# Optimization experiments

Measured on AMD Instinct MI355X. Metric: run time of the kernel, lower is better.

## Reference

```python
import jax, jax.numpy as jnp
import numpy as np

B = 4096  # number of graphs (segments)
H = 256   # hidden_aff = hidden_comp = hidden_prot
NEG = -1e30

def leaky(x):
    return jax.nn.leaky_relu(x, 0.1)

def _lin(key, fin, fout):
    k1, k2 = jax.random.split(key)
    lim = 1.0 / np.sqrt(fin)
    W = jax.random.uniform(k1, (fin, fout), jnp.float32, -lim, lim)
    b = jax.random.uniform(k2, (fout,), jnp.float32, -lim, lim)
    return W, b

def setup_inputs() -> dict:
    key = jax.random.key(0)
    ks = jax.random.split(key, 16)
    N = 262144
    comp_feature = jax.random.normal(ks[0], (N, H), jnp.float32)
    prot_feature = jax.random.normal(ks[1], (N, H), jnp.float32)
    batch_comp = jnp.sort(jax.random.randint(ks[2], (N,), 0, B, jnp.int32))
    batch_prot = jnp.sort(jax.random.randint(ks[3], (N,), 0, B, jnp.int32))
    c_aff_W, c_aff_b = _lin(ks[4], H, H)
    c_sup_W, c_sup_b = _lin(ks[5], H, H)
    p_aff_W, p_aff_b = _lin(ks[6], H, H)
    raw_W1, raw_b1 = _lin(ks[7], 3 * H, H)
    raw_W2, raw_b2 = _lin(ks[8], H, H)
    alpha_W1, alpha_b1 = _lin(ks[9], 3 * H, H)
    alpha_W2, alpha_b2 = _lin(ks[10], H, 1)
    out_W1, out_b1 = _lin(ks[11], H, H)
    out_W2, out_b2 = _lin(ks[12], H, 1)
    return dict(comp_feature=comp_feature, prot_feature=prot_feature,
                batch_comp=batch_comp, batch_prot=batch_prot,
                c_aff_W=c_aff_W, c_aff_b=c_aff_b, c_sup_W=c_sup_W, c_sup_b=c_sup_b,
                p_aff_W=p_aff_W, p_aff_b=p_aff_b,
                raw_W1=raw_W1, raw_b1=raw_b1, raw_W2=raw_W2, raw_b2=raw_b2,
                alpha_W1=alpha_W1, alpha_b1=alpha_b1, alpha_W2=alpha_W2, alpha_b2=alpha_b2,
                out_W1=out_W1, out_b1=out_b1, out_W2=out_W2, out_b2=out_b2)

def reference(comp_feature, prot_feature, batch_comp, batch_prot,
              c_aff_W, c_aff_b, c_sup_W, c_sup_b, p_aff_W, p_aff_b,
              raw_W1, raw_b1, raw_W2, raw_b2,
              alpha_W1, alpha_b1, alpha_W2, alpha_b2,
              out_W1, out_b1, out_W2, out_b2):
    comp_emb = leaky(comp_feature @ c_aff_W + c_aff_b)           # [N, H]
    prot_emb = leaky(prot_feature @ p_aff_W + p_aff_b)           # [N, H]
    prot_pool = jax.ops.segment_max(prot_emb, batch_prot, num_segments=B)  # [B, H]
    supe = jax.ops.segment_sum(leaky(comp_feature @ c_sup_W + c_sup_b),
                               batch_comp, num_segments=B)       # [B, H]
    feat = jnp.concatenate([comp_emb, supe[batch_comp], prot_pool[batch_comp]], axis=1)  # [N, 3H]
    raw = leaky(feat @ raw_W1 + raw_b1) @ raw_W2 + raw_b2        # [N, H]
    prealpha = leaky(feat @ alpha_W1 + alpha_b1) @ alpha_W2 + alpha_b2  # [N, 1]
    # scatter softmax over graphs
    seg_max = jax.ops.segment_max(prealpha, batch_comp, num_segments=B)
    a_exp = jnp.exp(prealpha - seg_max[batch_comp])
    a_sum = jax.ops.segment_sum(a_exp, batch_comp, num_segments=B) + 1e-6
    alpha = a_exp / a_sum[batch_comp]                            # [N, 1]
    vector = jax.ops.segment_sum(raw * alpha, batch_comp, num_segments=B)  # [B, H]
    affinity_pred = leaky(vector @ out_W1 + out_b1) @ out_W2 + out_b2      # [B, 1]
    return vector, alpha, affinity_pred
```

## Files before the change

kernel.cpp:

```cpp
#include <hip/hip_runtime.h>
#include <cstddef>
#include <cstdint>

#define HDIM 256
#define BSEG 4096

typedef __bf16 bf16x8 __attribute__((ext_vector_type(8)));
typedef float f32x4 __attribute__((ext_vector_type(4)));

__device__ __forceinline__ float leaky(float x) { return x >= 0.f ? x : 0.1f * x; }
__device__ __forceinline__ float bf2f(ushort u) {
    return __builtin_bit_cast(float, (uint32_t)u << 16);
}
__device__ __forceinline__ ushort f2bf(float f) {
    uint32_t x = __builtin_bit_cast(uint32_t, f);
    return (ushort)((x + 0x7fffu + ((x >> 16) & 1u)) >> 16);
}
__device__ __forceinline__ bf16x8 pack8(float4 a, float4 b) {
    union { ushort s[8]; bf16x8 v; } u;
    u.s[0] = f2bf(a.x); u.s[1] = f2bf(a.y); u.s[2] = f2bf(a.z); u.s[3] = f2bf(a.w);
    u.s[4] = f2bf(b.x); u.s[5] = f2bf(b.y); u.s[6] = f2bf(b.z); u.s[7] = f2bf(b.w);
    return u.v;
}
__device__ __forceinline__ void store_bf4(ushort* p, float v0, float v1, float v2, float v3) {
    ushort4 o; o.x = f2bf(v0); o.y = f2bf(v1); o.z = f2bf(v2); o.w = f2bf(v3);
    *(ushort4*)p = o;
}

__device__ __forceinline__ void gld16(const ushort* g, ushort* lds) {
    __builtin_amdgcn_global_load_lds(
        (const __attribute__((address_space(1))) uint32_t*)g,
        (__attribute__((address_space(3))) uint32_t*)lds, 16, 0, 0);
}

__global__ void seg_bounds_k(const int* __restrict__ bc, const int* __restrict__ bp,
                             int* __restrict__ sc, int* __restrict__ sp, int n, int nb)
{
    int t = blockIdx.x * blockDim.x + threadIdx.x;
    if (t >= 2 * (nb + 1)) return;
    bool isc = (t <= nb);
    const int* a = isc ? bc : bp;
    int v = isc ? t : t - (nb + 1);
    int lo = 0, hi = n;
    while (lo < hi) { int mid = (lo + hi) >> 1; if (a[mid] < v) lo = mid + 1; else hi = mid; }
    if (isc) sc[t] = lo; else sp[t - (nb + 1)] = lo;
}

__global__ __launch_bounds__(256) void wt_cast_all(
    const float* __restrict__ s0, const float* __restrict__ s1,
    const float* __restrict__ s2, const float* __restrict__ s3,
    const float* __restrict__ s4,
    ushort* __restrict__ d0, ushort* __restrict__ d1, ushort* __restrict__ d2,
    ushort* __restrict__ d3, ushort* __restrict__ d4)
{
    int m = blockIdx.x >> 4, tile = blockIdx.x & 15;
    const float* s = m == 0 ? s0 : m == 1 ? s1 : m == 2 ? s2 : m == 3 ? s3 : s4;
    ushort*      d = m == 0 ? d0 : m == 1 ? d1 : m == 2 ? d2 : m == 3 ? d3 : d4;
    int r0 = (tile >> 2) * 64, c0 = (tile & 3) * 64;
    __shared__ ushort t[64][72];
    int cc = threadIdx.x & 63, rr = threadIdx.x >> 6;
    for (int r = rr; r < 64; r += 4) t[cc][r] = f2bf(s[(size_t)(r0 + r) * 256 + c0 + cc]);
    __syncthreads();
    for (int r = rr; r < 64; r += 4) d[(size_t)(c0 + r) * 256 + r0 + cc] = t[r][cc];
}

template<bool LEAKYACT, bool ROWBIAS, bool AFP32, bool ALPHADOT, int YT>
__global__ __launch_bounds__(512) void mg3(
    const void* __restrict__ Av, const ushort* __restrict__ WT,
    const float* __restrict__ bias0, const float* __restrict__ bias1,
    const float* __restrict__ rt0, const float* __restrict__ rt1,
    const int* __restrict__ idx,
    ushort* __restrict__ out0, ushort* __restrict__ out1,
    const float* __restrict__ w2, float* __restrict__ pre)
{
    __shared__ __attribute__((aligned(16))) ushort Bs[2][256 * 32];
    __shared__ __attribute__((aligned(16))) ushort As[2][128 * 32];
    __shared__ float pb[128][4];

    const int tid = threadIdx.x;
    const int l = tid & 63, w = tid >> 6;

    const uint nwg = gridDim.x, orig = blockIdx.x;
    const uint swz = (orig & 7) * (nwg >> 3) + (orig >> 3);
    const int bx = (int)(swz / YT), cb = (int)(swz % YT);
    const int row0 = bx * 128, colb = cb * 256;

    const float*  Af = (const float*)Av;
    const ushort* Ah = (const ushort*)Av;

    const int sB0 = w * 128 + l;
    const int rB0 = sB0 >> 2,        rB1 = (sB0 + 64) >> 2;
    const int qB0 = (sB0 & 3) ^ ((rB0 >> 1) & 3), qB1 = ((sB0 + 64) & 3) ^ ((rB1 >> 1) & 3);
    const ushort* srcB0 = WT + (size_t)(colb + rB0) * HDIM + qB0 * 8;
    const ushort* srcB1 = WT + (size_t)(colb + rB1) * HDIM + qB1 * 8;
    const int srow = tid >> 2, sj = tid & 3;
    const int lj = sj ^ ((srow >> 1) & 3);
    const float*  fsrcA = Af + (size_t)(row0 + srow) * HDIM + lj * 8;
    const ushort* hsrcA = Ah + (size_t)(row0 + srow) * HDIM + lj * 8;

    const int wr = (w >> 2) * 64, wc = (w & 3) * 64;
    const int lr = l & 15, lt = l >> 4;

    f32x4 acc[4][4] = {};

#define STAGE_B(buf, k0) do { \
        gld16(srcB0 + (k0), &Bs[buf][sB0 * 8]); \
        gld16(srcB1 + (k0), &Bs[buf][(sB0 + 64) * 8]); \
    } while (0)

#define COMPUTE(buf) do { \
        bf16x8 af[4], bv[4]; \
        _Pragma("unroll") \
        for (int m = 0; m < 4; ++m) { \
            const int row = wr + m * 16 + lr; \
            const int q = lt ^ ((row >> 1) & 3); \
            af[m] = *(const bf16x8*)&As[buf][row * 32 + q * 8]; \
        } \
        _Pragma("unroll") \
        for (int n = 0; n < 4; ++n) { \
            const int brow = wc + n * 16 + lr; \
            const int q = lt ^ ((brow >> 1) & 3); \
            bv[n] = *(const bf16x8*)&Bs[buf][brow * 32 + q * 8]; \
        } \
        _Pragma("unroll") \
        for (int m = 0; m < 4; ++m) \
            _Pragma("unroll") \
            for (int n = 0; n < 4; ++n) \
                acc[m][n] = __builtin_amdgcn_mfma_f32_16x16x32_bf16(bv[n], af[m], acc[m][n], 0, 0, 0); \
    } while (0)

    int cur = 0;
    if (AFP32) {
        float4 av0, av1;
        av0 = *(const float4*)(fsrcA + 0);
        av1 = *(const float4*)(fsrcA + 4);
        STAGE_B(0, 0);
        *(bf16x8*)&As[0][tid * 8] = pack8(av0, av1);
        __syncthreads();
        #pragma unroll
        for (int t = 1; t < 8; ++t) {
            av0 = *(const float4*)(fsrcA + t * 32);
            av1 = *(const float4*)(fsrcA + t * 32 + 4);
            STAGE_B(cur ^ 1, t * 32);
            COMPUTE(cur);
            *(bf16x8*)&As[cur ^ 1][tid * 8] = pack8(av0, av1);
            __syncthreads();
            cur ^= 1;
        }
        COMPUTE(cur);
    } else {
        STAGE_B(0, 0);
        gld16(hsrcA, &As[0][tid * 8]);
        __syncthreads();
        #pragma unroll
        for (int t = 1; t < 8; ++t) {
            STAGE_B(cur ^ 1, t * 32);
            gld16(hsrcA + t * 32, &As[cur ^ 1][tid * 8]);
            COMPUTE(cur);
            __syncthreads();
            cur ^= 1;
        }
        COMPUTE(cur);
    }

#undef STAGE_B
#undef COMPUTE

    if (ALPHADOT && cb == 1) {
        #pragma unroll
        for (int m = 0; m < 4; ++m) {
            const int row = row0 + wr + m * 16 + lr;
            const float* rrow = rt1 + (size_t)idx[row] * HDIM;
            float p = 0.f;
            #pragma unroll
            for (int n = 0; n < 4; ++n) {
                const int c = wc + n * 16 + (lt << 2);
                float4 r4 = *(const float4*)&rrow[c];
                float4 w4 = *(const float4*)&w2[c];
                float v0 = acc[m][n][0] + r4.x, v1 = acc[m][n][1] + r4.y;
                float v2 = acc[m][n][2] + r4.z, v3 = acc[m][n][3] + r4.w;
                if (LEAKYACT) { v0 = leaky(v0); v1 = leaky(v1); v2 = leaky(v2); v3 = leaky(v3); }
                p += v0 * w4.x + v1 * w4.y + v2 * w4.z + v3 * w4.w;
            }
            p += __shfl_xor(p, 16);
            p += __shfl_xor(p, 32);
            if (lt == 0) pb[wr + m * 16 + lr][w & 3] = p;
        }
        __syncthreads();
        if (tid < 128) pre[row0 + tid] = pb[tid][0] + pb[tid][1] + pb[tid][2] + pb[tid][3];
    } else {
        const float* bias = (YT == 2 && cb == 1) ? bias1 : bias0;
        const float* rtab = (YT == 2 && cb == 1) ? rt1 : rt0;
        ushort* outp = (YT == 2 && cb == 1) ? out1 : out0;
        #pragma unroll
        for (int m = 0; m < 4; ++m) {
            const int row = row0 + wr + m * 16 + lr;
            const float* rrow = nullptr;
            if (ROWBIAS) rrow = rtab + (size_t)idx[row] * HDIM;
            #pragma unroll
            for (int n = 0; n < 4; ++n) {
                const int c = wc + n * 16 + (lt << 2);
                float v0 = acc[m][n][0], v1 = acc[m][n][1], v2 = acc[m][n][2], v3 = acc[m][n][3];
                if (bias) {
                    float4 b4 = *(const float4*)&bias[c];
                    v0 += b4.x; v1 += b4.y; v2 += b4.z; v3 += b4.w;
                }
                if (ROWBIAS) {
                    float4 r4 = *(const float4*)&rrow[c];
                    v0 += r4.x; v1 += r4.y; v2 += r4.z; v3 += r4.w;
                }
                if (LEAKYACT) { v0 = leaky(v0); v1 = leaky(v1); v2 = leaky(v2); v3 = leaky(v3); }
                store_bf4(&outp[(size_t)row * HDIM + c], v0, v1, v2, v3);
            }
        }
    }
}

__global__ __launch_bounds__(256) void gemm64_2(
    const float* __restrict__ A, const float* __restrict__ A2,
    const float* __restrict__ Wb_r, const float* __restrict__ Wc_r, const float* __restrict__ bias_r,
    const float* __restrict__ Wb_a, const float* __restrict__ Wc_a, const float* __restrict__ bias_a,
    float* __restrict__ Cr, float* __restrict__ Ca)
{
    const int K = HDIM, NO = HDIM;
    const float* W  = blockIdx.z ? Wb_a : Wb_r;
    const float* W2 = blockIdx.z ? Wc_a : Wc_r;
    const float* bias = blockIdx.z ? bias_a : bias_r;
    float* C = blockIdx.z ? Ca : Cr;

    __shared__ float As [16][68];
    __shared__ float Bs [16][68];
    __shared__ float As2[16][68];
    __shared__ float Bs2[16][68];

    const int tid = threadIdx.x;
    const int tx = tid & 15, ty = tid >> 4;
    const int row0 = blockIdx.x * 64, col0 = blockIdx.y * 64;

    const int lr = tid >> 2;
    const int lk = (tid & 3) << 2;
    const int bk = tid >> 4;
    const int bj = (tid & 15) << 2;

    float acc[4][4] = {};

    for (int k0 = 0; k0 < K; k0 += 16) {
        float4 a4 = *(const float4*)&A[(size_t)(row0 + lr) * K + k0 + lk];
        As[lk + 0][lr] = a4.x; As[lk + 1][lr] = a4.y;
        As[lk + 2][lr] = a4.z; As[lk + 3][lr] = a4.w;
        *(float4*)&Bs[bk][bj] = *(const float4*)&W[(size_t)(k0 + bk) * NO + col0 + bj];
        float4 c4 = *(const float4*)&A2[(size_t)(row0 + lr) * K + k0 + lk];
        As2[lk + 0][lr] = c4.x; As2[lk + 1][lr] = c4.y;
        As2[lk + 2][lr] = c4.z; As2[lk + 3][lr] = c4.w;
        *(float4*)&Bs2[bk][bj] = *(const float4*)&W2[(size_t)(k0 + bk) * NO + col0 + bj];
        __syncthreads();
        #pragma unroll
        for (int kk = 0; kk < 16; ++kk) {
            float4 av = *(const float4*)&As[kk][ty << 2];
            float4 bv = *(const float4*)&Bs[kk][tx << 2];
            float a_[4] = {av.x, av.y, av.z, av.w};
            float b_[4] = {bv.x, bv.y, bv.z, bv.w};
            #pragma unroll
            for (int i = 0; i < 4; ++i)
                #pragma unroll
                for (int j = 0; j < 4; ++j)
                    acc[i][j] += a_[i] * b_[j];
            float4 av2 = *(const float4*)&As2[kk][ty << 2];
            float4 bv2 = *(const float4*)&Bs2[kk][tx << 2];
            float c_[4] = {av2.x, av2.y, av2.z, av2.w};
            float d_[4] = {bv2.x, bv2.y, bv2.z, bv2.w};
            #pragma unroll
            for (int i = 0; i < 4; ++i)
                #pragma unroll
                for (int j = 0; j < 4; ++j)
                    acc[i][j] += c_[i] * d_[j];
        }
        __syncthreads();
    }

    #pragma unroll
    for (int i = 0; i < 4; ++i) {
        int row = row0 + (ty << 2) + i;
        float vv[4];
        #pragma unroll
        for (int j = 0; j < 4; ++j) {
            int col = col0 + (tx << 2) + j;
            vv[j] = acc[i][j] + bias[col];
        }
        float4 o; o.x = vv[0]; o.y = vv[1]; o.z = vv[2]; o.w = vv[3];
        *(float4*)&C[(size_t)row * NO + col0 + (tx << 2)] = o;
    }
}

template<bool ISMAX>
__global__ __launch_bounds__(256) void seg_reduce8(const ushort* __restrict__ in,
        const int* __restrict__ starts, float* __restrict__ out)
{
    __shared__ float part[8][HDIM];
    const int b = blockIdx.x, tid = threadIdx.x;
    const int sub = tid & 31, r = tid >> 5;
    const int s = starts[b], e = starts[b + 1];
    float a[8];
    #pragma unroll
    for (int j = 0; j < 8; ++j) a[j] = ISMAX ? -INFINITY : 0.f;
    for (int i = s + r; i < e; i += 8) {
        uint4 v = *(const uint4*)&in[(size_t)i * HDIM + sub * 8];
        float f[8] = { bf2f((ushort)v.x), bf2f((ushort)(v.x >> 16)),
                       bf2f((ushort)v.y), bf2f((ushort)(v.y >> 16)),
                       bf2f((ushort)v.z), bf2f((ushort)(v.z >> 16)),
                       bf2f((ushort)v.w), bf2f((ushort)(v.w >> 16)) };
        #pragma unroll
        for (int j = 0; j < 8; ++j) a[j] = ISMAX ? fmaxf(a[j], f[j]) : (a[j] + f[j]);
    }
    #pragma unroll
    for (int j = 0; j < 8; ++j) part[r][sub * 8 + j] = a[j];
    __syncthreads();
    float res = part[0][tid];
    #pragma unroll
    for (int j = 1; j < 8; ++j) res = ISMAX ? fmaxf(res, part[j][tid]) : (res + part[j][tid]);
    out[(size_t)b * HDIM + tid] = res;
}

__global__ __launch_bounds__(64) void seg_softmax_k(const float* __restrict__ pre,
        const int* __restrict__ starts, float* __restrict__ alpha, float* __restrict__ sa)
{
    int b = blockIdx.x, lane = threadIdx.x;
    int s = starts[b], e = starts[b + 1];
    float m = -INFINITY;
    for (int i = s + lane; i < e; i += 64) m = fmaxf(m, pre[i]);
    #pragma unroll
    for (int off = 32; off; off >>= 1) m = fmaxf(m, __shfl_xor(m, off));
    float S = 0.f;
    for (int i = s + lane; i < e; i += 64) S += expf(pre[i] - m);
    #pragma unroll
    for (int off = 32; off; off >>= 1) S += __shfl_xor(S, off);
    float denom = S + 1e-6f;
    if (lane == 0) sa[b] = S / denom;
    for (int i = s + lane; i < e; i += 64) alpha[i] = expf(pre[i] - m) / denom;
}

__global__ __launch_bounds__(256) void seg_wsum8(const ushort* __restrict__ raw,
        const float* __restrict__ alpha, const int* __restrict__ starts,
        float* __restrict__ vec)
{
    __shared__ float part[8][HDIM];
    const int b = blockIdx.x, tid = threadIdx.x;
    const int sub = tid & 31, r = tid >> 5;
    const int s = starts[b], e = starts[b + 1];
    float a[8] = {};
    for (int i = s + r; i < e; i += 8) {
        float al = alpha[i];
        uint4 v = *(const uint4*)&raw[(size_t)i * HDIM + sub * 8];
        a[0] += bf2f((ushort)v.x) * al;        a[1] += bf2f((ushort)(v.x >> 16)) * al;
        a[2] += bf2f((ushort)v.y) * al;        a[3] += bf2f((ushort)(v.y >> 16)) * al;
        a[4] += bf2f((ushort)v.z) * al;        a[5] += bf2f((ushort)(v.z >> 16)) * al;
        a[6] += bf2f((ushort)v.w) * al;        a[7] += bf2f((ushort)(v.w >> 16)) * al;
    }
    #pragma unroll
    for (int j = 0; j < 8; ++j) part[r][sub * 8 + j] = a[j];
    __syncthreads();
    float res = 0.f;
    #pragma unroll
    for (int j = 0; j < 8; ++j) res += part[j][tid];
    vec[(size_t)b * HDIM + tid] = res;
}

__global__ __launch_bounds__(256) void final_k(
    const float* __restrict__ hw, const float* __restrict__ sa,
    const float* __restrict__ W2r, const float* __restrict__ rb2,
    const float* __restrict__ oW1, const float* __restrict__ ob1,
    const float* __restrict__ oW2, const float* __restrict__ ob2,
    float* __restrict__ out_vec, float* __restrict__ out_aff)
{
    __shared__ float v[HDIM];
    __shared__ float vecs[HDIM];
    __shared__ float red[4];
    int b = blockIdx.x, t = threadIdx.x;
    v[t] = hw[(size_t)b * HDIM + t];
    __syncthreads();
    float a = rb2[t] * sa[b];
    #pragma unroll 8
    for (int k = 0; k < HDIM; ++k) a += v[k] * W2r[(size_t)k * HDIM + t];
    out_vec[(size_t)b * HDIM + t] = a;
    vecs[t] = a;
    __syncthreads();
    float h = ob1[t];
    #pragma unroll 8
    for (int k = 0; k < HDIM; ++k) h += vecs[k] * oW1[(size_t)k * HDIM + t];
    h = leaky(h);
    float p = h * oW2[t];
    #pragma unroll
    for (int off = 32; off; off >>= 1) p += __shfl_down(p, off);
    int lane = t & 63, wid = t >> 6;
    if (lane == 0) red[wid] = p;
    __syncthreads();
    if (t == 0) out_aff[b] = red[0] + red[1] + red[2] + red[3] + ob2[0];
}

extern "C" void kernel_launch(void* const* d_in, const int* in_sizes, int n_in,
                              void* d_out, int out_size, void* d_ws, size_t ws_size,
                              hipStream_t stream)
{
    const int N = in_sizes[2];
    const int H = HDIM;
    const int B = BSEG;

    const float* comp   = (const float*)d_in[0];
    const float* prot   = (const float*)d_in[1];
    const int*   bc     = (const int*)d_in[2];
    const int*   bp     = (const int*)d_in[3];
    const float* c_aff_W = (const float*)d_in[4];
    const float* c_aff_b = (const float*)d_in[5];
    const float* c_sup_W = (const float*)d_in[6];
    const float* c_sup_b = (const float*)d_in[7];
    const float* p_aff_W = (const float*)d_in[8];
    const float* p_aff_b = (const float*)d_in[9];
    const float* raw_W1  = (const float*)d_in[10];
    const float* raw_b1  = (const float*)d_in[11];
    const float* raw_W2  = (const float*)d_in[12];
    const float* raw_b2  = (const float*)d_in[13];
    const float* alpha_W1 = (const float*)d_in[14];
    const float* alpha_b1 = (const float*)d_in[15];
    const float* alpha_W2 = (const float*)d_in[16];
    const float* out_W1  = (const float*)d_in[18];
    const float* out_b1  = (const float*)d_in[19];
    const float* out_W2  = (const float*)d_in[20];
    const float* out_b2  = (const float*)d_in[21];

    const size_t NBIG = (size_t)N * H;
    const size_t SSEG = (size_t)B * H;

    char* p = (char*)d_ws;
    ushort* e1 = (ushort*)p; p += NBIG * 2;
    ushort* e2 = (ushort*)p; p += NBIG * 2;
    ushort* e3 = (ushort*)p; p += NBIG * 2;
    float* supe = (float*)p;  p += SSEG * 4;
    float* pool = (float*)p;  p += SSEG * 4;
    float* gr   = (float*)p;  p += SSEG * 4;
    float* ga   = (float*)p;  p += SSEG * 4;
    float* hw   = (float*)p;  p += SSEG * 4;
    float* sa   = (float*)p;  p += (size_t)B * 4;
    float* pre  = (float*)p;  p += (size_t)N * 4;
    ushort* WT1 = (ushort*)p; p += (size_t)512 * 256 * 2;
    ushort* WTp = (ushort*)p; p += (size_t)256 * 256 * 2;
    ushort* WT2 = (ushort*)p; p += (size_t)512 * 256 * 2;
    int* sc = (int*)p; p += (size_t)(B + 1) * 4;
    int* sp = (int*)p; p += (size_t)(B + 1) * 4;
    if ((size_t)(p - (char*)d_ws) > ws_size) return;

    ushort* h1 = e3;

    float* out_vec   = (float*)d_out;
    float* out_alpha = out_vec + SSEG;
    float* out_aff   = out_alpha + N;

    dim3 blk(256), blk5(512);

    seg_bounds_k<<<(2 * (B + 1) + 255) / 256, blk, 0, stream>>>(bc, bp, sc, sp, N, B);
    wt_cast_all<<<5 * 16, blk, 0, stream>>>(
        c_aff_W, c_sup_W, p_aff_W, raw_W1, alpha_W1,
        WT1, WT1 + 65536, WTp, WT2, WT2 + 65536);

    mg3<true, false, true, false, 2><<<dim3(N / 128 * 2), blk5, 0, stream>>>(
        comp, WT1, c_aff_b, c_sup_b, nullptr, nullptr, nullptr, e1, e2, nullptr, nullptr);
    mg3<true, false, true, false, 1><<<dim3(N / 128), blk5, 0, stream>>>(
        prot, WTp, p_aff_b, nullptr, nullptr, nullptr, nullptr, e3, nullptr, nullptr, nullptr);
    seg_reduce8<false><<<B, blk, 0, stream>>>(e2, sc, supe);
    seg_reduce8<true ><<<B, blk, 0, stream>>>(e3, sp, pool);
    gemm64_2<<<dim3(B / 64, 4, 2), blk, 0, stream>>>(supe, pool,
        raw_W1 + H * H, raw_W1 + 2 * H * H, raw_b1,
        alpha_W1 + H * H, alpha_W1 + 2 * H * H, alpha_b1, gr, ga);
    mg3<true, true, false, true, 2><<<dim3(N / 128 * 2), blk5, 0, stream>>>(
        e1, WT2, nullptr, nullptr, gr, ga, bc, h1, nullptr, alpha_W2, pre);
    seg_softmax_k<<<B, dim3(64), 0, stream>>>(pre, sc, out_alpha, sa);
    seg_wsum8<<<B, blk, 0, stream>>>(h1, out_alpha, sc, hw);
    final_k<<<B, blk, 0, stream>>>(hw, sa, raw_W2, raw_b2,
        out_W1, out_b1, out_W2, out_b2, out_vec, out_aff);
}
```

Measured before the change: 686.3 us.

## Enlarge GEMM row tile to 256 rows per block with 8x4 MFMA accumulators

Doubles the M tile of the MFMA GEMM kernel from 128 to 256 rows, so each wave computes 128x64 outputs (8x4 accumulator tiles) and each loaded B tile is reused across twice as many rows. A staging now uses two 16-byte slots per thread, and the grid is halved. The aim is higher arithmetic intensity and less redundant weight traffic. The cost is more registers (128 accumulator floats) and more LDS, which lowers occupancy and may cause spilling.

Result: slower. 700.2 us (+2.0%).

```diff
diff --git a/kernel.cpp b/kernel.cpp
--- a/kernel.cpp
+++ b/kernel.cpp
@@ -65,7 +65,7 @@
 }
 
 template<bool LEAKYACT, bool ROWBIAS, bool AFP32, bool ALPHADOT, int YT>
-__global__ __launch_bounds__(512) void mg3(
+__global__ __launch_bounds__(512) void mg8(
     const void* __restrict__ Av, const ushort* __restrict__ WT,
     const float* __restrict__ bias0, const float* __restrict__ bias1,
     const float* __restrict__ rt0, const float* __restrict__ rt1,
@@ -74,8 +74,8 @@
     const float* __restrict__ w2, float* __restrict__ pre)
 {
     __shared__ __attribute__((aligned(16))) ushort Bs[2][256 * 32];
-    __shared__ __attribute__((aligned(16))) ushort As[2][128 * 32];
-    __shared__ float pb[128][4];
+    __shared__ __attribute__((aligned(16))) ushort As[2][256 * 32];
+    __shared__ float pb[256][4];
 
     const int tid = threadIdx.x;
     const int l = tid & 63, w = tid >> 6;
@@ -83,35 +83,57 @@
     const uint nwg = gridDim.x, orig = blockIdx.x;
     const uint swz = (orig & 7) * (nwg >> 3) + (orig >> 3);
     const int bx = (int)(swz / YT), cb = (int)(swz % YT);
-    const int row0 = bx * 128, colb = cb * 256;
+    const int row0 = bx * 256, colb = cb * 256;
 
     const float*  Af = (const float*)Av;
     const ushort* Ah = (const ushort*)Av;
 
-    const int sB0 = w * 128 + l;
-    const int rB0 = sB0 >> 2,        rB1 = (sB0 + 64) >> 2;
-    const int qB0 = (sB0 & 3) ^ ((rB0 >> 1) & 3), qB1 = ((sB0 + 64) & 3) ^ ((rB1 >> 1) & 3);
+    const int s0 = tid, s1 = tid + 512;
+    const int rB0 = s0 >> 2, rB1 = s1 >> 2;
+    const int qB0 = (s0 & 3) ^ ((rB0 >> 1) & 3), qB1 = (s1 & 3) ^ ((rB1 >> 1) & 3);
     const ushort* srcB0 = WT + (size_t)(colb + rB0) * HDIM + qB0 * 8;
     const ushort* srcB1 = WT + (size_t)(colb + rB1) * HDIM + qB1 * 8;
-    const int srow = tid >> 2, sj = tid & 3;
-    const int lj = sj ^ ((srow >> 1) & 3);
-    const float*  fsrcA = Af + (size_t)(row0 + srow) * HDIM + lj * 8;
-    const ushort* hsrcA = Ah + (size_t)(row0 + srow) * HDIM + lj * 8;
-
-    const int wr = (w >> 2) * 64, wc = (w & 3) * 64;
+    const int rA0 = s0 >> 2, rA1 = s1 >> 2;
+    const int qA0 = (s0 & 3) ^ ((rA0 >> 1) & 3), qA1 = (s1 & 3) ^ ((rA1 >> 1) & 3);
+    const float*  fsrcA0 = Af + (size_t)(row0 + rA0) * HDIM + qA0 * 8;
+    const float*  fsrcA1 = Af + (size_t)(row0 + rA1) * HDIM + qA1 * 8;
+    const ushort* hsrcA0 = Ah + (size_t)(row0 + rA0) * HDIM + qA0 * 8;
+    const ushort* hsrcA1 = Ah + (size_t)(row0 + rA1) * HDIM + qA1 * 8;
+
+    const int wr = (w >> 2) * 128, wc = (w & 3) * 64;
     const int lr = l & 15, lt = l >> 4;
 
-    f32x4 acc[4][4] = {};
+    f32x4 acc[8][4] = {};
+    float4 fa[4];
+    bf16x8 hb[2];
+    (void)hb;
 
 #define STAGE_B(buf, k0) do { \
-        gld16(srcB0 + (k0), &Bs[buf][sB0 * 8]); \
-        gld16(srcB1 + (k0), &Bs[buf][(sB0 + 64) * 8]); \
+        gld16(srcB0 + (k0), &Bs[buf][s0 * 8]); \
+        gld16(srcB1 + (k0), &Bs[buf][s1 * 8]); \
     } while (0)
 
+#define LOAD_A_F(k0) do { \
+        fa[0] = *(const float4*)(fsrcA0 + (k0)); \
+        fa[1] = *(const float4*)(fsrcA0 + (k0) + 4); \
+        fa[2] = *(const float4*)(fsrcA1 + (k0)); \
+        fa[3] = *(const float4*)(fsrcA1 + (k0) + 4); \
+    } while (0)
+
+#define WRITE_A(buf) do { \
+        *(bf16x8*)&As[buf][s0 * 8] = pack8(fa[0], fa[1]); \
+        *(bf16x8*)&As[buf][s1 * 8] = pack8(fa[2], fa[3]); \
+    } while (0)
+
+#define STAGE_A_H(buf, k0) do { \
+        gld16(hsrcA0 + (k0), &As[buf][s0 * 8]); \
+        gld16(hsrcA1 + (k0), &As[buf][s1 * 8]); \
+    } while (0)
+
 #define COMPUTE(buf) do { \
-        bf16x8 af[4], bv[4]; \
+        bf16x8 af[8], bv[4]; \
         _Pragma("unroll") \
-        for (int m = 0; m < 4; ++m) { \
+        for (int m = 0; m < 8; ++m) { \
             const int row = wr + m * 16 + lr; \
             const int q = lt ^ ((row >> 1) & 3); \
             af[m] = *(const bf16x8*)&As[buf][row * 32 + q * 8]; \
@@ -123,52 +145,44 @@
             bv[n] = *(const bf16x8*)&Bs[buf][brow * 32 + q * 8]; \
         } \
         _Pragma("unroll") \
-        for (int m = 0; m < 4; ++m) \
+        for (int m = 0; m < 8; ++m) \
             _Pragma("unroll") \
             for (int n = 0; n < 4; ++n) \
                 acc[m][n] = __builtin_amdgcn_mfma_f32_16x16x32_bf16(bv[n], af[m], acc[m][n], 0, 0, 0); \
     } while (0)
 
-    int cur = 0;
     if (AFP32) {
-        float4 av0, av1;
-        av0 = *(const float4*)(fsrcA + 0);
-        av1 = *(const float4*)(fsrcA + 4);
+        LOAD_A_F(0);
         STAGE_B(0, 0);
-        *(bf16x8*)&As[0][tid * 8] = pack8(av0, av1);
+        WRITE_A(0);
         __syncthreads();
         #pragma unroll
-        for (int t = 1; t < 8; ++t) {
-            av0 = *(const float4*)(fsrcA + t * 32);
-            av1 = *(const float4*)(fsrcA + t * 32 + 4);
-            STAGE_B(cur ^ 1, t * 32);
-            COMPUTE(cur);
-            *(bf16x8*)&As[cur ^ 1][tid * 8] = pack8(av0, av1);
-            __syncthreads();
-            cur ^= 1;
-        }
-        COMPUTE(cur);
+        for (int t = 0; t < 8; ++t) {
+            if (t < 7) { STAGE_B((t + 1) & 1, (t + 1) * 32); LOAD_A_F((t + 1) * 32); }
+            COMPUTE(t & 1);
+            if (t < 7) { WRITE_A((t + 1) & 1); __syncthreads(); }
+        }
     } else {
         STAGE_B(0, 0);
-        gld16(hsrcA, &As[0][tid * 8]);
+        STAGE_A_H(0, 0);
         __syncthreads();
         #pragma unroll
-        for (int t = 1; t < 8; ++t) {
-            STAGE_B(cur ^ 1, t * 32);
-            gld16(hsrcA + t * 32, &As[cur ^ 1][tid * 8]);
-            COMPUTE(cur);
-            __syncthreads();
-            cur ^= 1;
-        }
-        COMPUTE(cur);
+        for (int t = 0; t < 8; ++t) {
+            if (t < 7) { STAGE_B((t + 1) & 1, (t + 1) * 32); STAGE_A_H((t + 1) & 1, (t + 1) * 32); }
+            COMPUTE(t & 1);
+            if (t < 7) __syncthreads();
+        }
     }
 
 #undef STAGE_B
+#undef LOAD_A_F
+#undef WRITE_A
+#undef STAGE_A_H
 #undef COMPUTE
 
     if (ALPHADOT && cb == 1) {
         #pragma unroll
-        for (int m = 0; m < 4; ++m) {
+        for (int m = 0; m < 8; ++m) {
             const int row = row0 + wr + m * 16 + lr;
             const float* rrow = rt1 + (size_t)idx[row] * HDIM;
             float p = 0.f;
@@ -187,13 +201,13 @@
             if (lt == 0) pb[wr + m * 16 + lr][w & 3] = p;
         }
         __syncthreads();
-        if (tid < 128) pre[row0 + tid] = pb[tid][0] + pb[tid][1] + pb[tid][2] + pb[tid][3];
+        if (tid < 256) pre[row0 + tid] = pb[tid][0] + pb[tid][1] + pb[tid][2] + pb[tid][3];
     } else {
         const float* bias = (YT == 2 && cb == 1) ? bias1 : bias0;
         const float* rtab = (YT == 2 && cb == 1) ? rt1 : rt0;
         ushort* outp = (YT == 2 && cb == 1) ? out1 : out0;
         #pragma unroll
-        for (int m = 0; m < 4; ++m) {
+        for (int m = 0; m < 8; ++m) {
             const int row = row0 + wr + m * 16 + lr;
             const float* rrow = nullptr;
             if (ROWBIAS) rrow = rtab + (size_t)idx[row] * HDIM;
@@ -461,16 +475,16 @@
         c_aff_W, c_sup_W, p_aff_W, raw_W1, alpha_W1,
         WT1, WT1 + 65536, WTp, WT2, WT2 + 65536);
 
-    mg3<true, false, true, false, 2><<<dim3(N / 128 * 2), blk5, 0, stream>>>(
+    mg8<true, false, true, false, 2><<<dim3(N / 256 * 2), blk5, 0, stream>>>(
         comp, WT1, c_aff_b, c_sup_b, nullptr, nullptr, nullptr, e1, e2, nullptr, nullptr);
-    mg3<true, false, true, false, 1><<<dim3(N / 128), blk5, 0, stream>>>(
+    mg8<true, false, true, false, 1><<<dim3(N / 256), blk5, 0, stream>>>(
         prot, WTp, p_aff_b, nullptr, nullptr, nullptr, nullptr, e3, nullptr, nullptr, nullptr);
     seg_reduce8<false><<<B, blk, 0, stream>>>(e2, sc, supe);
     seg_reduce8<true ><<<B, blk, 0, stream>>>(e3, sp, pool);
     gemm64_2<<<dim3(B / 64, 4, 2), blk, 0, stream>>>(supe, pool,
         raw_W1 + H * H, raw_W1 + 2 * H * H, raw_b1,
         alpha_W1 + H * H, alpha_W1 + 2 * H * H, alpha_b1, gr, ga);
-    mg3<true, true, false, true, 2><<<dim3(N / 128 * 2), blk5, 0, stream>>>(
+    mg8<true, true, false, true, 2><<<dim3(N / 256 * 2), blk5, 0, stream>>>(
         e1, WT2, nullptr, nullptr, gr, ga, bc, h1, nullptr, alpha_W2, pre);
     seg_softmax_k<<<B, dim3(64), 0, stream>>>(pre, sc, out_alpha, sa);
     seg_wsum8<<<B, blk, 0, stream>>>(h1, out_alpha, sc, hw);
```

## Fuse comp_emb GEMM into raw/alpha GEMM, keeping embedding tile in LDS

Applied to the files above, without the earlier changes.

Comp_emb is no longer written to global memory as e1 and read back. A new fused kernel computes the comp_aff GEMM per 128-row tile, stores the leaky bf16 result in shared memory, then runs both the raw and alpha second-layer GEMMs from LDS. This removes a full N×H bf16 write and read. The cost is that comp_feature is re-read (the sup GEMM now runs separately), B operands are read directly from global without LDS staging, and the kernel uses a large LDS footprint (about 80KB), which lowers occupancy.

Result: slower. 790.2 us (+15.1%).

```diff
diff --git a/kernel.cpp b/kernel.cpp
--- a/kernel.cpp
+++ b/kernel.cpp
@@ -64,18 +64,14 @@
     for (int r = rr; r < 64; r += 4) d[(size_t)(c0 + r) * 256 + r0 + cc] = t[r][cc];
 }
 
-template<bool LEAKYACT, bool ROWBIAS, bool AFP32, bool ALPHADOT, int YT>
+template<bool LEAKYACT, bool AFP32, int YT>
 __global__ __launch_bounds__(512) void mg3(
     const void* __restrict__ Av, const ushort* __restrict__ WT,
-    const float* __restrict__ bias0, const float* __restrict__ bias1,
-    const float* __restrict__ rt0, const float* __restrict__ rt1,
-    const int* __restrict__ idx,
-    ushort* __restrict__ out0, ushort* __restrict__ out1,
-    const float* __restrict__ w2, float* __restrict__ pre)
+    const float* __restrict__ bias0,
+    ushort* __restrict__ out0)
 {
     __shared__ __attribute__((aligned(16))) ushort Bs[2][256 * 32];
     __shared__ __attribute__((aligned(16))) ushort As[2][128 * 32];
-    __shared__ float pb[128][4];
 
     const int tid = threadIdx.x;
     const int l = tid & 63, w = tid >> 6;
@@ -84,6 +80,7 @@
     const uint swz = (orig & 7) * (nwg >> 3) + (orig >> 3);
     const int bx = (int)(swz / YT), cb = (int)(swz % YT);
     const int row0 = bx * 128, colb = cb * 256;
+    (void)colb;
 
     const float*  Af = (const float*)Av;
     const ushort* Ah = (const ushort*)Av;
@@ -166,21 +163,169 @@
 #undef STAGE_B
 #undef COMPUTE
 
-    if (ALPHADOT && cb == 1) {
+    #pragma unroll
+    for (int m = 0; m < 4; ++m) {
+        const int row = row0 + wr + m * 16 + lr;
+        #pragma unroll
+        for (int n = 0; n < 4; ++n) {
+            const int c = wc + n * 16 + (lt << 2);
+            float v0 = acc[m][n][0], v1 = acc[m][n][1], v2 = acc[m][n][2], v3 = acc[m][n][3];
+            float4 b4 = *(const float4*)&bias0[c];
+            v0 += b4.x; v1 += b4.y; v2 += b4.z; v3 += b4.w;
+            if (LEAKYACT) { v0 = leaky(v0); v1 = leaky(v1); v2 = leaky(v2); v3 = leaky(v3); }
+            store_bf4(&out0[(size_t)row * HDIM + c], v0, v1, v2, v3);
+        }
+    }
+}
+
+__global__ __launch_bounds__(512) void mgfused(
+    const float* __restrict__ Af, const ushort* __restrict__ WTa,
+    const float* __restrict__ abias,
+    const ushort* __restrict__ WT2,
+    const float* __restrict__ gr, const float* __restrict__ ga,
+    const int* __restrict__ idx, const float* __restrict__ w2,
+    ushort* __restrict__ h1, float* __restrict__ pre)
+{
+    __shared__ __attribute__((aligned(16))) ushort As[2][128 * 32];
+    __shared__ __attribute__((aligned(16))) ushort eL[8][128 * 32];
+    float (*pb)[4] = (float (*)[4])As;
+
+    const int tid = threadIdx.x;
+    const int l = tid & 63, w = tid >> 6;
+    const uint nwg = gridDim.x, orig = blockIdx.x;
+    const uint swz = (orig & 7) * (nwg >> 3) + (orig >> 3);
+    const int row0 = (int)swz * 128;
+
+    const int srow = tid >> 2, sj = tid & 3;
+    const int lj = sj ^ ((srow >> 1) & 3);
+    const float* fsrcA = Af + (size_t)(row0 + srow) * HDIM + lj * 8;
+
+    const int wr = (w >> 2) * 64, wc = (w & 3) * 64;
+    const int lr = l & 15, lt = l >> 4;
+
+    f32x4 acc[4][4] = {};
+
+    {
+        float4 av0 = *(const float4*)(fsrcA);
+        float4 av1 = *(const float4*)(fsrcA + 4);
+        *(bf16x8*)&As[0][tid * 8] = pack8(av0, av1);
+        __syncthreads();
+        #pragma unroll
+        for (int t = 0; t < 8; ++t) {
+            if (t < 7) {
+                av0 = *(const float4*)(fsrcA + (t + 1) * 32);
+                av1 = *(const float4*)(fsrcA + (t + 1) * 32 + 4);
+            }
+            bf16x8 af[4], bv[4];
+            #pragma unroll
+            for (int m = 0; m < 4; ++m) {
+                const int row = wr + m * 16 + lr;
+                const int q = lt ^ ((row >> 1) & 3);
+                af[m] = *(const bf16x8*)&As[t & 1][row * 32 + q * 8];
+            }
+            #pragma unroll
+            for (int n = 0; n < 4; ++n)
+                bv[n] = *(const bf16x8*)&WTa[(size_t)(wc + n * 16 + lr) * HDIM + t * 32 + lt * 8];
+            #pragma unroll
+            for (int m = 0; m < 4; ++m)
+                #pragma unroll
+                for (int n = 0; n < 4; ++n)
+                    acc[m][n] = __builtin_amdgcn_mfma_f32_16x16x32_bf16(bv[n], af[m], acc[m][n], 0, 0, 0);
+            if (t < 7) {
+                *(bf16x8*)&As[(t + 1) & 1][tid * 8] = pack8(av0, av1);
+                __syncthreads();
+            }
+        }
+    }
+    #pragma unroll
+    for (int m = 0; m < 4; ++m) {
+        const int r = wr + m * 16 + lr;
+        #pragma unroll
+        for (int n = 0; n < 4; ++n) {
+            const int c = wc + n * 16 + (lt << 2);
+            float4 b4 = *(const float4*)&abias[c];
+            float v0 = leaky(acc[m][n][0] + b4.x);
+            float v1 = leaky(acc[m][n][1] + b4.y);
+            float v2 = leaky(acc[m][n][2] + b4.z);
+            float v3 = leaky(acc[m][n][3] + b4.w);
+            const int ks = c >> 5, o = c & 31;
+            const int s = (o >> 3) ^ ((r >> 1) & 3);
+            ushort4 u; u.x = f2bf(v0); u.y = f2bf(v1); u.z = f2bf(v2); u.w = f2bf(v3);
+            *(ushort4*)&eL[ks][r * 32 + s * 8 + (o & 7)] = u;
+        }
+    }
+    __syncthreads();
+
+    {
+        f32x4 hacc[4][4] = {};
+        #pragma unroll
+        for (int ks = 0; ks < 8; ++ks) {
+            bf16x8 af[4], bv[4];
+            #pragma unroll
+            for (int m = 0; m < 4; ++m) {
+                const int row = wr + m * 16 + lr;
+                const int q = lt ^ ((row >> 1) & 3);
+                af[m] = *(const bf16x8*)&eL[ks][row * 32 + q * 8];
+            }
+            #pragma unroll
+            for (int n = 0; n < 4; ++n)
+                bv[n] = *(const bf16x8*)&WT2[(size_t)(wc + n * 16 + lr) * HDIM + ks * 32 + lt * 8];
+            #pragma unroll
+            for (int m = 0; m < 4; ++m)
+                #pragma unroll
+                for (int n = 0; n < 4; ++n)
+                    hacc[m][n] = __builtin_amdgcn_mfma_f32_16x16x32_bf16(bv[n], af[m], hacc[m][n], 0, 0, 0);
+        }
         #pragma unroll
         for (int m = 0; m < 4; ++m) {
             const int row = row0 + wr + m * 16 + lr;
-            const float* rrow = rt1 + (size_t)idx[row] * HDIM;
+            const float* rrow = gr + (size_t)idx[row] * HDIM;
+            #pragma unroll
+            for (int n = 0; n < 4; ++n) {
+                const int c = wc + n * 16 + (lt << 2);
+                float4 r4 = *(const float4*)&rrow[c];
+                store_bf4(&h1[(size_t)row * HDIM + c],
+                          leaky(hacc[m][n][0] + r4.x), leaky(hacc[m][n][1] + r4.y),
+                          leaky(hacc[m][n][2] + r4.z), leaky(hacc[m][n][3] + r4.w));
+            }
+        }
+    }
+
+    {
+        f32x4 aacc[4][4] = {};
+        #pragma unroll
+        for (int ks = 0; ks < 8; ++ks) {
+            bf16x8 af[4], bv[4];
+            #pragma unroll
+            for (int m = 0; m < 4; ++m) {
+                const int row = wr + m * 16 + lr;
+                const int q = lt ^ ((row >> 1) & 3);
+                af[m] = *(const bf16x8*)&eL[ks][row * 32 + q * 8];
+            }
+            #pragma unroll
+            for (int n = 0; n < 4; ++n)
+                bv[n] = *(const bf16x8*)&WT2[(size_t)(256 + wc + n * 16 + lr) * HDIM + ks * 32 + lt * 8];
+            #pragma unroll
+            for (int m = 0; m < 4; ++m)
+                #pragma unroll
+                for (int n = 0; n < 4; ++n)
+                    aacc[m][n] = __builtin_amdgcn_mfma_f32_16x16x32_bf16(bv[n], af[m], aacc[m][n], 0, 0, 0);
+        }
+        __syncthreads();
+        #pragma unroll
+        for (int m = 0; m < 4; ++m) {
+            const int row = row0 + wr + m * 16 + lr;
+            const float* rrow = ga + (size_t)idx[row] * HDIM;
             float p = 0.f;
             #pragma unroll
             for (int n = 0; n < 4; ++n) {
                 const int c = wc + n * 16 + (lt << 2);
                 float4 r4 = *(const float4*)&rrow[c];
                 float4 w4 = *(const float4*)&w2[c];
-                float v0 = acc[m][n][0] + r4.x, v1 = acc[m][n][1] + r4.y;
-                float v2 = acc[m][n][2] + r4.z, v3 = acc[m][n][3] + r4.w;
-                if (LEAKYACT) { v0 = leaky(v0); v1 = leaky(v1); v2 = leaky(v2); v3 = leaky(v3); }
-                p += v0 * w4.x + v1 * w4.y + v2 * w4.z + v3 * w4.w;
+                p += leaky(aacc[m][n][0] + r4.x) * w4.x;
+                p += leaky(aacc[m][n][1] + r4.y) * w4.y;
+                p += leaky(aacc[m][n][2] + r4.z) * w4.z;
+                p += leaky(aacc[m][n][3] + r4.w) * w4.w;
             }
             p += __shfl_xor(p, 16);
             p += __shfl_xor(p, 32);
@@ -188,31 +333,6 @@
         }
         __syncthreads();
         if (tid < 128) pre[row0 + tid] = pb[tid][0] + pb[tid][1] + pb[tid][2] + pb[tid][3];
-    } else {
-        const float* bias = (YT == 2 && cb == 1) ? bias1 : bias0;
-        const float* rtab = (YT == 2 && cb == 1) ? rt1 : rt0;
-        ushort* outp = (YT == 2 && cb == 1) ? out1 : out0;
-        #pragma unroll
-        for (int m = 0; m < 4; ++m) {
-            const int row = row0 + wr + m * 16 + lr;
-            const float* rrow = nullptr;
-            if (ROWBIAS) rrow = rtab + (size_t)idx[row] * HDIM;
-            #pragma unroll
-            for (int n = 0; n < 4; ++n) {
-                const int c = wc + n * 16 + (lt << 2);
-                float v0 = acc[m][n][0], v1 = acc[m][n][1], v2 = acc[m][n][2], v3 = acc[m][n][3];
-                if (bias) {
-                    float4 b4 = *(const float4*)&bias[c];
-                    v0 += b4.x; v1 += b4.y; v2 += b4.z; v3 += b4.w;
-                }
-                if (ROWBIAS) {
-                    float4 r4 = *(const float4*)&rrow[c];
-                    v0 += r4.x; v1 += r4.y; v2 += r4.z; v3 += r4.w;
-                }
-                if (LEAKYACT) { v0 = leaky(v0); v1 = leaky(v1); v2 = leaky(v2); v3 = leaky(v3); }
-                store_bf4(&outp[(size_t)row * HDIM + c], v0, v1, v2, v3);
-            }
-        }
     }
 }
 
@@ -431,7 +551,6 @@
     const size_t SSEG = (size_t)B * H;
 
     char* p = (char*)d_ws;
-    ushort* e1 = (ushort*)p; p += NBIG * 2;
     ushort* e2 = (ushort*)p; p += NBIG * 2;
     ushort* e3 = (ushort*)p; p += NBIG * 2;
     float* supe = (float*)p;  p += SSEG * 4;
@@ -441,7 +560,8 @@
     float* hw   = (float*)p;  p += SSEG * 4;
     float* sa   = (float*)p;  p += (size_t)B * 4;
     float* pre  = (float*)p;  p += (size_t)N * 4;
-    ushort* WT1 = (ushort*)p; p += (size_t)512 * 256 * 2;
+    ushort* WTa = (ushort*)p; p += (size_t)256 * 256 * 2;
+    ushort* WTs = (ushort*)p; p += (size_t)256 * 256 * 2;
     ushort* WTp = (ushort*)p; p += (size_t)256 * 256 * 2;
     ushort* WT2 = (ushort*)p; p += (size_t)512 * 256 * 2;
     int* sc = (int*)p; p += (size_t)(B + 1) * 4;
@@ -459,19 +579,17 @@
     seg_bounds_k<<<(2 * (B + 1) + 255) / 256, blk, 0, stream>>>(bc, bp, sc, sp, N, B);
     wt_cast_all<<<5 * 16, blk, 0, stream>>>(
         c_aff_W, c_sup_W, p_aff_W, raw_W1, alpha_W1,
-        WT1, WT1 + 65536, WTp, WT2, WT2 + 65536);
-
-    mg3<true, false, true, false, 2><<<dim3(N / 128 * 2), blk5, 0, stream>>>(
-        comp, WT1, c_aff_b, c_sup_b, nullptr, nullptr, nullptr, e1, e2, nullptr, nullptr);
-    mg3<true, false, true, false, 1><<<dim3(N / 128), blk5, 0, stream>>>(
-        prot, WTp, p_aff_b, nullptr, nullptr, nullptr, nullptr, e3, nullptr, nullptr, nullptr);
+        WTa, WTs, WTp, WT2, WT2 + 65536);
+
+    mg3<true, true, 1><<<dim3(N / 128), blk5, 0, stream>>>(comp, WTs, c_sup_b, e2);
+    mg3<true, true, 1><<<dim3(N / 128), blk5, 0, stream>>>(prot, WTp, p_aff_b, e3);
     seg_reduce8<false><<<B, blk, 0, stream>>>(e2, sc, supe);
     seg_reduce8<true ><<<B, blk, 0, stream>>>(e3, sp, pool);
     gemm64_2<<<dim3(B / 64, 4, 2), blk, 0, stream>>>(supe, pool,
         raw_W1 + H * H, raw_W1 + 2 * H * H, raw_b1,
         alpha_W1 + H * H, alpha_W1 + 2 * H * H, alpha_b1, gr, ga);
-    mg3<true, true, false, true, 2><<<dim3(N / 128 * 2), blk5, 0, stream>>>(
-        e1, WT2, nullptr, nullptr, gr, ga, bc, h1, nullptr, alpha_W2, pre);
+    mgfused<<<dim3(N / 128), blk5, 0, stream>>>(
+        comp, WTa, c_aff_b, WT2, gr, ga, bc, alpha_W2, h1, pre);
     seg_softmax_k<<<B, dim3(64), 0, stream>>>(pre, sc, out_alpha, sa);
     seg_wsum8<<<B, blk, 0, stream>>>(h1, out_alpha, sc, hw);
     final_k<<<B, blk, 0, stream>>>(hw, sa, raw_W2, raw_b2,
```

## Fuse segment sum/max pooling into GEMM epilogues via shuffle scans and atomics

Applied to the files above, without the earlier changes.

The c_sup and p_aff GEMM epilogues now reduce rows within each 16-lane group using segmented shuffle scans. They then issue atomicAdd for the sum and an integer-keyed atomicMax for the max into per-segment buffers, instead of writing bf16 intermediates and running separate seg_reduce8 kernels. This removes two full N×H bf16 writes and reads, and it drops the sum and max reduction launches. In exchange it adds many global atomics, an init kernel and an unmap kernel, and the float atomicAdd order becomes nondeterministic.

Result: no change. 690.7 us (+0.6%).

```diff
diff --git a/kernel.cpp b/kernel.cpp
--- a/kernel.cpp
+++ b/kernel.cpp
@@ -26,11 +26,14 @@
     ushort4 o; o.x = f2bf(v0); o.y = f2bf(v1); o.z = f2bf(v2); o.w = f2bf(v3);
     *(ushort4*)p = o;
 }
-
 __device__ __forceinline__ void gld16(const ushort* g, ushort* lds) {
     __builtin_amdgcn_global_load_lds(
         (const __attribute__((address_space(1))) uint32_t*)g,
         (__attribute__((address_space(3))) uint32_t*)lds, 16, 0, 0);
+}
+__device__ __forceinline__ int fkey(float f) {
+    int b = __builtin_bit_cast(int, f);
+    return b >= 0 ? b : b ^ 0x7fffffff;
 }
 
 __global__ void seg_bounds_k(const int* __restrict__ bc, const int* __restrict__ bp,
@@ -64,15 +67,33 @@
     for (int r = rr; r < 64; r += 4) d[(size_t)(c0 + r) * 256 + r0 + cc] = t[r][cc];
 }
 
-template<bool LEAKYACT, bool ROWBIAS, bool AFP32, bool ALPHADOT, int YT>
-__global__ __launch_bounds__(512) void mg3(
+__global__ __launch_bounds__(256) void init_red_k(float* __restrict__ supe, int* __restrict__ pooli)
+{
+    int i = blockIdx.x * 256 + threadIdx.x;
+    supe[i] = 0.f;
+    pooli[i] = (int)0x807fffff;
+}
+__global__ __launch_bounds__(256) void unmap_pool_k(const int* __restrict__ pooli, float* __restrict__ pool)
+{
+    int i = blockIdx.x * 256 + threadIdx.x;
+    int k = pooli[i];
+    int b = k >= 0 ? k : k ^ 0x7fffffff;
+    pool[i] = __builtin_bit_cast(float, b);
+}
+
+template<int MODE>
+__global__ __launch_bounds__(512) void mgx(
     const void* __restrict__ Av, const ushort* __restrict__ WT,
     const float* __restrict__ bias0, const float* __restrict__ bias1,
     const float* __restrict__ rt0, const float* __restrict__ rt1,
     const int* __restrict__ idx,
-    ushort* __restrict__ out0, ushort* __restrict__ out1,
+    ushort* __restrict__ out0,
+    float* __restrict__ supe, int* __restrict__ pooli,
     const float* __restrict__ w2, float* __restrict__ pre)
 {
+    constexpr bool AFP32 = (MODE != 2);
+    constexpr int YT = (MODE == 1) ? 1 : 2;
+
     __shared__ __attribute__((aligned(16))) ushort Bs[2][256 * 32];
     __shared__ __attribute__((aligned(16))) ushort As[2][128 * 32];
     __shared__ float pb[128][4];
@@ -166,7 +187,56 @@
 #undef STAGE_B
 #undef COMPUTE
 
-    if (ALPHADOT && cb == 1) {
+    if (MODE == 0 && cb == 0) {
+        #pragma unroll
+        for (int m = 0; m < 4; ++m) {
+            const int row = row0 + wr + m * 16 + lr;
+            #pragma unroll
+            for (int n = 0; n < 4; ++n) {
+                const int c = wc + n * 16 + (lt << 2);
+                float4 b4 = *(const float4*)&bias0[c];
+                store_bf4(&out0[(size_t)row * HDIM + c],
+                          leaky(acc[m][n][0] + b4.x), leaky(acc[m][n][1] + b4.y),
+                          leaky(acc[m][n][2] + b4.z), leaky(acc[m][n][3] + b4.w));
+            }
+        }
+    } else if (MODE == 0 || MODE == 1) {
+        const float* bias = (MODE == 0) ? bias1 : bias0;
+        #pragma unroll
+        for (int m = 0; m < 4; ++m) {
+            const int row = row0 + wr + m * 16 + lr;
+            const int seg = idx[row];
+            bool take[4];
+            #pragma unroll
+            for (int k = 0; k < 4; ++k) {
+                int so = __shfl_up(seg, 1 << k, 16);
+                take[k] = (lr >= (1 << k)) && (so == seg);
+            }
+            int segdn = __shfl_down(seg, 1, 16);
+            const bool last = (lr == 15) || (segdn != seg);
+            #pragma unroll
+            for (int n = 0; n < 4; ++n) {
+                const int c = wc + n * 16 + (lt << 2);
+                float4 b4 = *(const float4*)&bias[c];
+                float v[4] = { leaky(acc[m][n][0] + b4.x), leaky(acc[m][n][1] + b4.y),
+                               leaky(acc[m][n][2] + b4.z), leaky(acc[m][n][3] + b4.w) };
+                #pragma unroll
+                for (int j = 0; j < 4; ++j) {
+                    float x = v[j];
+                    #pragma unroll
+                    for (int k = 0; k < 4; ++k) {
+                        float o = __shfl_up(x, 1 << k, 16);
+                        if (MODE == 0) { if (take[k]) x += o; }
+                        else           { if (take[k]) x = fmaxf(x, o); }
+                    }
+                    if (last) {
+                        if (MODE == 0) atomicAdd(&supe[(size_t)seg * HDIM + c + j], x);
+                        else           atomicMax(&pooli[(size_t)seg * HDIM + c + j], fkey(x));
+                    }
+                }
+            }
+        }
+    } else if (MODE == 2 && cb == 1) {
         #pragma unroll
         for (int m = 0; m < 4; ++m) {
             const int row = row0 + wr + m * 16 + lr;
@@ -177,10 +247,10 @@
                 const int c = wc + n * 16 + (lt << 2);
                 float4 r4 = *(const float4*)&rrow[c];
                 float4 w4 = *(const float4*)&w2[c];
-                float v0 = acc[m][n][0] + r4.x, v1 = acc[m][n][1] + r4.y;
-                float v2 = acc[m][n][2] + r4.z, v3 = acc[m][n][3] + r4.w;
-                if (LEAKYACT) { v0 = leaky(v0); v1 = leaky(v1); v2 = leaky(v2); v3 = leaky(v3); }
-                p += v0 * w4.x + v1 * w4.y + v2 * w4.z + v3 * w4.w;
+                p += leaky(acc[m][n][0] + r4.x) * w4.x;
+                p += leaky(acc[m][n][1] + r4.y) * w4.y;
+                p += leaky(acc[m][n][2] + r4.z) * w4.z;
+                p += leaky(acc[m][n][3] + r4.w) * w4.w;
             }
             p += __shfl_xor(p, 16);
             p += __shfl_xor(p, 32);
@@ -189,28 +259,17 @@
         __syncthreads();
         if (tid < 128) pre[row0 + tid] = pb[tid][0] + pb[tid][1] + pb[tid][2] + pb[tid][3];
     } else {
-        const float* bias = (YT == 2 && cb == 1) ? bias1 : bias0;
-        const float* rtab = (YT == 2 && cb == 1) ? rt1 : rt0;
-        ushort* outp = (YT == 2 && cb == 1) ? out1 : out0;
         #pragma unroll
         for (int m = 0; m < 4; ++m) {
             const int row = row0 + wr + m * 16 + lr;
-            const float* rrow = nullptr;
-            if (ROWBIAS) rrow = rtab + (size_t)idx[row] * HDIM;
+            const float* rrow = rt0 + (size_t)idx[row] * HDIM;
             #pragma unroll
             for (int n = 0; n < 4; ++n) {
                 const int c = wc + n * 16 + (lt << 2);
-                float v0 = acc[m][n][0], v1 = acc[m][n][1], v2 = acc[m][n][2], v3 = acc[m][n][3];
-                if (bias) {
-                    float4 b4 = *(const float4*)&bias[c];
-                    v0 += b4.x; v1 += b4.y; v2 += b4.z; v3 += b4.w;
-                }
-                if (ROWBIAS) {
-                    float4 r4 = *(const float4*)&rrow[c];
-                    v0 += r4.x; v1 += r4.y; v2 += r4.z; v3 += r4.w;
-                }
-                if (LEAKYACT) { v0 = leaky(v0); v1 = leaky(v1); v2 = leaky(v2); v3 = leaky(v3); }
-                store_bf4(&outp[(size_t)row * HDIM + c], v0, v1, v2, v3);
+                float4 r4 = *(const float4*)&rrow[c];
+                store_bf4(&out0[(size_t)row * HDIM + c],
+                          leaky(acc[m][n][0] + r4.x), leaky(acc[m][n][1] + r4.y),
+                          leaky(acc[m][n][2] + r4.z), leaky(acc[m][n][3] + r4.w));
             }
         }
     }
@@ -290,35 +349,6 @@
         float4 o; o.x = vv[0]; o.y = vv[1]; o.z = vv[2]; o.w = vv[3];
         *(float4*)&C[(size_t)row * NO + col0 + (tx << 2)] = o;
     }
-}
-
-template<bool ISMAX>
-__global__ __launch_bounds__(256) void seg_reduce8(const ushort* __restrict__ in,
-        const int* __restrict__ starts, float* __restrict__ out)
-{
-    __shared__ float part[8][HDIM];
-    const int b = blockIdx.x, tid = threadIdx.x;
-    const int sub = tid & 31, r = tid >> 5;
-    const int s = starts[b], e = starts[b + 1];
-    float a[8];
-    #pragma unroll
-    for (int j = 0; j < 8; ++j) a[j] = ISMAX ? -INFINITY : 0.f;
-    for (int i = s + r; i < e; i += 8) {
-        uint4 v = *(const uint4*)&in[(size_t)i * HDIM + sub * 8];
-        float f[8] = { bf2f((ushort)v.x), bf2f((ushort)(v.x >> 16)),
-                       bf2f((ushort)v.y), bf2f((ushort)(v.y >> 16)),
-                       bf2f((ushort)v.z), bf2f((ushort)(v.z >> 16)),
-                       bf2f((ushort)v.w), bf2f((ushort)(v.w >> 16)) };
-        #pragma unroll
-        for (int j = 0; j < 8; ++j) a[j] = ISMAX ? fmaxf(a[j], f[j]) : (a[j] + f[j]);
-    }
-    #pragma unroll
-    for (int j = 0; j < 8; ++j) part[r][sub * 8 + j] = a[j];
-    __syncthreads();
-    float res = part[0][tid];
-    #pragma unroll
-    for (int j = 1; j < 8; ++j) res = ISMAX ? fmaxf(res, part[j][tid]) : (res + part[j][tid]);
-    out[(size_t)b * HDIM + tid] = res;
 }
 
 __global__ __launch_bounds__(64) void seg_softmax_k(const float* __restrict__ pre,
@@ -432,10 +462,10 @@
 
     char* p = (char*)d_ws;
     ushort* e1 = (ushort*)p; p += NBIG * 2;
-    ushort* e2 = (ushort*)p; p += NBIG * 2;
-    ushort* e3 = (ushort*)p; p += NBIG * 2;
+    ushort* h1 = (ushort*)p; p += NBIG * 2;
     float* supe = (float*)p;  p += SSEG * 4;
     float* pool = (float*)p;  p += SSEG * 4;
+    int*  pooli = (int*)p;    p += SSEG * 4;
     float* gr   = (float*)p;  p += SSEG * 4;
     float* ga   = (float*)p;  p += SSEG * 4;
     float* hw   = (float*)p;  p += SSEG * 4;
@@ -448,8 +478,6 @@
     int* sp = (int*)p; p += (size_t)(B + 1) * 4;
     if ((size_t)(p - (char*)d_ws) > ws_size) return;
 
-    ushort* h1 = e3;
-
     float* out_vec   = (float*)d_out;
     float* out_alpha = out_vec + SSEG;
     float* out_aff   = out_alpha + N;
@@ -460,18 +488,18 @@
     wt_cast_all<<<5 * 16, blk, 0, stream>>>(
         c_aff_W, c_sup_W, p_aff_W, raw_W1, alpha_W1,
         WT1, WT1 + 65536, WTp, WT2, WT2 + 65536);
-
-    mg3<true, false, true, false, 2><<<dim3(N / 128 * 2), blk5, 0, stream>>>(
-        comp, WT1, c_aff_b, c_sup_b, nullptr, nullptr, nullptr, e1, e2, nullptr, nullptr);
-    mg3<true, false, true, false, 1><<<dim3(N / 128), blk5, 0, stream>>>(
-        prot, WTp, p_aff_b, nullptr, nullptr, nullptr, nullptr, e3, nullptr, nullptr, nullptr);
-    seg_reduce8<false><<<B, blk, 0, stream>>>(e2, sc, supe);
-    seg_reduce8<true ><<<B, blk, 0, stream>>>(e3, sp, pool);
+    init_red_k<<<(int)(SSEG / 256), blk, 0, stream>>>(supe, pooli);
+
+    mgx<0><<<dim3(N / 128 * 2), blk5, 0, stream>>>(
+        comp, WT1, c_aff_b, c_sup_b, nullptr, nullptr, bc, e1, supe, nullptr, nullptr, nullptr);
+    mgx<1><<<dim3(N / 128), blk5, 0, stream>>>(
+        prot, WTp, p_aff_b, nullptr, nullptr, nullptr, bp, nullptr, nullptr, pooli, nullptr, nullptr);
+    unmap_pool_k<<<(int)(SSEG / 256), blk, 0, stream>>>(pooli, pool);
     gemm64_2<<<dim3(B / 64, 4, 2), blk, 0, stream>>>(supe, pool,
         raw_W1 + H * H, raw_W1 + 2 * H * H, raw_b1,
         alpha_W1 + H * H, alpha_W1 + 2 * H * H, alpha_b1, gr, ga);
-    mg3<true, true, false, true, 2><<<dim3(N / 128 * 2), blk5, 0, stream>>>(
-        e1, WT2, nullptr, nullptr, gr, ga, bc, h1, nullptr, alpha_W2, pre);
+    mgx<2><<<dim3(N / 128 * 2), blk5, 0, stream>>>(
+        e1, WT2, nullptr, nullptr, gr, ga, bc, h1, nullptr, nullptr, alpha_W2, pre);
     seg_softmax_k<<<B, dim3(64), 0, stream>>>(pre, sc, out_alpha, sa);
     seg_wsum8<<<B, blk, 0, stream>>>(h1, out_alpha, sc, hw);
     final_k<<<B, blk, 0, stream>>>(hw, sa, raw_W2, raw_b2,
```
